# Performance work log

Hardware: AMD Instinct MI355X
Metric: run time of the kernel (lower is better)

The kernel has to match this reference:

```python
import jax, jax.numpy as jnp
import numpy as np

N_NODES = 100_000
N_EDGES = 1_600_000
N_GRAPHS = 512
IN_C, HID_C, OUT_C = 17, 64, 32


def setup_inputs() -> dict:
    key = jax.random.key(0)
    ks = jax.random.split(key, 12)
    x = jax.random.normal(ks[0], (N_NODES, IN_C), dtype=jnp.float32)
    edge_index = jax.random.randint(ks[1], (2, N_EDGES), 0, N_NODES, dtype=jnp.int64)
    batch = jnp.sort(jax.random.randint(ks[2], (N_NODES,), 0, N_GRAPHS, dtype=jnp.int64))
    def lin(k, fan_in, fan_out):
        s = 1.0 / np.sqrt(fan_in)
        kw, kb = jax.random.split(k)
        W = jax.random.uniform(kw, (fan_in, fan_out), minval=-s, maxval=s, dtype=jnp.float32)
        b = jax.random.uniform(kb, (fan_out,), minval=-s, maxval=s, dtype=jnp.float32)
        return W, b
    W1, b1 = lin(ks[3], IN_C, HID_C)      # GCNConv 1
    W2, b2 = lin(ks[4], HID_C, OUT_C)     # GCNConv 2
    Wf1, bf1 = lin(ks[5], OUT_C, OUT_C)   # fc1
    Wf2, bf2 = lin(ks[6], OUT_C, OUT_C)   # fc2
    return {"x": x, "edge_index": edge_index, "batch": batch,
            "W1": W1, "b1": b1, "W2": W2, "b2": b2,
            "Wf1": Wf1, "bf1": bf1, "Wf2": Wf2, "bf2": bf2}


def _gcn_conv(x, src, dst, norm, W, b, n_nodes):
    # PyG GCNConv: h = x @ W; out_i = sum_{j->i} norm_ij * h_j; out += bias
    h = x @ W                                   # [N, d_out]
    msg = h[src] * norm[:, None]                # gather + scale [E+N, d_out]
    out = jax.ops.segment_sum(msg, dst, num_segments=n_nodes)
    return out + b


def reference(x, edge_index, batch, W1, b1, W2, b2, Wf1, bf1, Wf2, bf2):
    n = x.shape[0]
    loops = jnp.arange(n, dtype=edge_index.dtype)
    src = jnp.concatenate([edge_index[0], loops])  # add self loops
    dst = jnp.concatenate([edge_index[1], loops])
    # symmetric normalization: deg^-1/2[src] * deg^-1/2[dst]
    deg = jax.ops.segment_sum(jnp.ones_like(dst, dtype=x.dtype), dst, num_segments=n)
    dinv = jnp.where(deg > 0, 1.0 / jnp.sqrt(deg), 0.0)
    norm = dinv[src] * dinv[dst]

    h = jax.nn.relu(_gcn_conv(x, src, dst, norm, W1, b1, n))
    h = _gcn_conv(h, src, dst, norm, W2, b2, n)

    # global mean pool over graphs
    cnt = jax.ops.segment_sum(jnp.ones((n,), dtype=h.dtype), batch, num_segments=N_GRAPHS)
    pooled = jax.ops.segment_sum(h, batch, num_segments=N_GRAPHS) / jnp.clip(cnt, 1.0)[:, None]

    out = jax.nn.relu(pooled @ Wf1 + bf1)
    out = out @ Wf2 + bf2
    return out  # [N_GRAPHS, OUT_C]
```

## Files before the change

### kernel.cpp

```cpp
#include <hip/hip_runtime.h>

#define IN_C 17
#define HID  64
#define OUTC 32

#define CH   8192
#define TA   512
#define NBP  512
#define BCAP 5632
#define BS_BLKS 8

typedef __attribute__((ext_vector_type(2))) float f2;
typedef __attribute__((ext_vector_type(8))) short bf16x8;
typedef __attribute__((ext_vector_type(4))) float f32x4;
__device__ __forceinline__ f2 mkf2(float x, float y) { f2 r; r.x = x; r.y = y; return r; }

__device__ __forceinline__ unsigned short f2bf(float f) {
    unsigned u = __float_as_uint(f);
    u += 0x7fffu + ((u >> 16) & 1u);
    return (unsigned short)(u >> 16);
}
__device__ __forceinline__ float bflo(unsigned u) { return __uint_as_float(u << 16); }
__device__ __forceinline__ float bfhi(unsigned u) { return __uint_as_float(u & 0xffff0000u); }

__global__ __launch_bounds__(TA) void k_binA(const int* __restrict__ src,
        const int* __restrict__ dst, int E,
        int* __restrict__ outbuf, int* __restrict__ cntmat, int* __restrict__ offmat,
        const float* __restrict__ W2, uint4* __restrict__ w2frag,
        float* __restrict__ pool, int poolN) {
    __shared__ int cnt[NBP];
    __shared__ int off[NBP];
    __shared__ int stage[CH];
    int t = threadIdx.x;
    for (int i = (int)(blockIdx.x * TA + t); i < poolN; i += (int)(gridDim.x * TA))
        pool[i] = 0.f;
    if (blockIdx.x == 0 && t < 256) {
        int f = t >> 6, l = t & 63;
        int kt = f >> 1, nt = f & 1;
        int kbase = kt * 32 + (l >> 4) * 8;
        int c = nt * 16 + (l & 15);
        unsigned short v[8];
#pragma unroll
        for (int j = 0; j < 8; ++j) v[j] = f2bf(W2[(kbase + j) * OUTC + c]);
        uint4 o;
        o.x = (unsigned)v[0] | ((unsigned)v[1] << 16);
        o.y = (unsigned)v[2] | ((unsigned)v[3] << 16);
        o.z = (unsigned)v[4] | ((unsigned)v[5] << 16);
        o.w = (unsigned)v[6] | ((unsigned)v[7] << 16);
        w2frag[f * 64 + l] = o;
    }
    long base = (long)blockIdx.x * CH;
    int nE = (int)(E - base); if (nE > CH) nE = CH;
    cnt[t] = 0;
    __syncthreads();
    int bk[16], pk[16], rk[16];
#pragma unroll
    for (int j = 0; j < 16; ++j) {
        int idx = t + j * TA;
        if (idx < nE) {
            long e = base + idx;
            int d = __builtin_nontemporal_load(&dst[e]);
            int s = __builtin_nontemporal_load(&src[e]);
            int b = d >> 8;
            bk[j] = b;
            pk[j] = s | ((d & 255) << 17);
            rk[j] = atomicAdd(&cnt[b], 1);
        } else bk[j] = -1;
    }
    __syncthreads();
    int c = cnt[t];
    off[t] = c;
    __syncthreads();
    int inc = c;
    for (int s = 1; s < NBP; s <<= 1) {
        int add = (t >= s) ? off[t - s] : 0;
        __syncthreads();
        inc += add; off[t] = inc;
        __syncthreads();
    }
    int excl = inc - c;
    __syncthreads();
    off[t] = excl;
    __syncthreads();
#pragma unroll
    for (int j = 0; j < 16; ++j)
        if (bk[j] >= 0) stage[off[bk[j]] + rk[j]] = pk[j];
    __syncthreads();
    for (int i = t; i < nE; i += TA) outbuf[base + i] = stage[i];
    cntmat[blockIdx.x * NBP + t] = c;
    offmat[blockIdx.x * NBP + t] = excl;
}

__global__ __launch_bounds__(NBP) void k_bsum1(const int* __restrict__ cntmat,
        int nblkA, int* __restrict__ part) {
    int t = threadIdx.x, b = blockIdx.x;
    int per = (nblkA + BS_BLKS - 1) / BS_BLKS;
    int i0 = b * per, i1 = min(i0 + per, nblkA);
    int s = 0;
    for (int i = i0; i < i1; ++i) s += cntmat[i * NBP + t];
    part[b * NBP + t] = s;
}

__global__ __launch_bounds__(NBP) void k_bsum2(const int* __restrict__ part,
        int* __restrict__ bbase) {
    __shared__ int sh[NBP];
    int t = threadIdx.x;
    int s = 0;
#pragma unroll
    for (int i = 0; i < BS_BLKS; ++i) s += part[i * NBP + t];
    sh[t] = s;
    __syncthreads();
    int inc = s;
    for (int st = 1; st < NBP; st <<= 1) {
        int add = (t >= st) ? sh[t - st] : 0;
        __syncthreads();
        inc += add; sh[t] = inc;
        __syncthreads();
    }
    bbase[t] = inc - s;
}

__global__ __launch_bounds__(TA) void k_binB(const int* __restrict__ outbuf,
        const int* __restrict__ cntmat, const int* __restrict__ offmat,
        const int* __restrict__ bbase, int nblkA, int N,
        int* __restrict__ csr, int2* __restrict__ meta,
        const float* __restrict__ x, unsigned* __restrict__ xs16h,
        unsigned short* __restrict__ xs17h) {
    __shared__ int segc[256], sego[256], segs[256];
    __shared__ int ndeg[256], noff[256];
    __shared__ int stage[BCAP];
    int t = threadIdx.x, b = blockIdx.x;
    if (t < 256) {
        int cc = 0, ss = 0;
        if (t < nblkA) { cc = cntmat[t * NBP + b]; ss = offmat[t * NBP + b]; }
        segc[t] = cc; segs[t] = ss; sego[t] = cc;
        ndeg[t] = 0;
    }
    __syncthreads();
    {
        int c = (t < 256) ? sego[t] : 0;
        int inc = c;
        for (int s = 1; s < 256; s <<= 1) {
            int add = (t < 256 && t >= s) ? sego[t - s] : 0;
            __syncthreads();
            if (t < 256) { inc += add; sego[t] = inc; }
            __syncthreads();
        }
        if (t < 256) sego[t] = inc - c;
    }
    __syncthreads();
    int wave = t >> 6, lane = t & 63;
    for (int i = wave; i < nblkA; i += TA / 64) {
        int c = segc[i], so = sego[i];
        long gs = (long)i * CH + segs[i];
        for (int l = lane; l < c; l += 64) {
            int p = so + l;
            if (p < BCAP) stage[p] = __builtin_nontemporal_load(&outbuf[gs + l]);
        }
    }
    __syncthreads();
    int T = sego[255] + segc[255];
    if (T > BCAP) T = BCAP;
    int mypk[11], myrk[11], ne = 0;
    for (int k = t; k < T; k += TA) {
        int p = stage[k];
        int l = (p >> 17) & 255;
        myrk[ne] = atomicAdd(&ndeg[l], 1);
        mypk[ne] = p;
        ne++;
    }
    __syncthreads();
    {
        int c = (t < 256) ? ndeg[t] : 0;
        if (t < 256) noff[t] = c;
        __syncthreads();
        int inc = c;
        for (int s = 1; s < 256; s <<= 1) {
            int add = (t < 256 && t >= s) ? noff[t - s] : 0;
            __syncthreads();
            if (t < 256) { inc += add; noff[t] = inc; }
            __syncthreads();
        }
        if (t < 256) noff[t] = inc - c;
    }
    __syncthreads();
    int gb = bbase[b];
    int n0 = b << 8;
    if (t < 256 && n0 + t < N) {
        int n = n0 + t;
        meta[n] = make_int2(gb + noff[t], ndeg[t]);
        float dinv = rsqrtf((float)(ndeg[t] + 1));
        const float* xr = x + (size_t)n * IN_C;
        unsigned* xo = xs16h + (size_t)n * 8;
#pragma unroll
        for (int w2 = 0; w2 < 8; ++w2) {
            unsigned lo = f2bf(xr[2 * w2] * dinv);
            unsigned hi = f2bf(xr[2 * w2 + 1] * dinv);
            xo[w2] = lo | (hi << 16);
        }
        xs17h[n] = f2bf(xr[16] * dinv);
    }
    for (int j = 0; j < ne; ++j) {
        int p = mypk[j];
        int l = (p >> 17) & 255;
        csr[gb + noff[l] + myrk[j]] = p & 0x1FFFF;
    }
}

__global__ __launch_bounds__(256) void k_gather1(
        const uint4* __restrict__ xs16v, const unsigned short* __restrict__ xs17h,
        const int* __restrict__ csr, const int2* __restrict__ meta,
        const float* __restrict__ W1, const float* __restrict__ b1,
        const uint4* __restrict__ w2frag, unsigned char* __restrict__ hs2b, int N) {
    __shared__ __align__(16) float aggx[16][20];
    __shared__ float dinv_sh[16];
    __shared__ __align__(16) float h1sh[16][68];

    int tid = threadIdx.x;
    int n0 = blockIdx.x * 16;
    int ch = tid & 63;
    float w1r[IN_C];
#pragma unroll
    for (int k = 0; k < IN_C; ++k) w1r[k] = W1[k * HID + ch];
    float b1v = b1[ch];

    int ln = tid >> 4, sl = tid & 15;
    int n = n0 + ln;
    f2 acc[8];
#pragma unroll
    for (int j = 0; j < 8; ++j) acc[j] = mkf2(0.f, 0.f);
    float a17 = 0.f;
    if (n < N) {
        int2 m = meta[n];
        int start = m.x, cnt = m.y, end = start + cnt;
        auto body = [&](int s) {
            uint4 v0 = xs16v[(size_t)s * 2];
            uint4 v1 = xs16v[(size_t)s * 2 + 1];
            acc[0] += mkf2(bflo(v0.x), bfhi(v0.x));
            acc[1] += mkf2(bflo(v0.y), bfhi(v0.y));
            acc[2] += mkf2(bflo(v0.z), bfhi(v0.z));
            acc[3] += mkf2(bflo(v0.w), bfhi(v0.w));
            acc[4] += mkf2(bflo(v1.x), bfhi(v1.x));
            acc[5] += mkf2(bflo(v1.y), bfhi(v1.y));
            acc[6] += mkf2(bflo(v1.z), bfhi(v1.z));
            acc[7] += mkf2(bflo(v1.w), bfhi(v1.w));
            a17 += bflo((unsigned)xs17h[s]);
        };
        for (int k = start + sl; k < end; k += 16)
            body(__builtin_nontemporal_load(&csr[k]));
        if (sl == 0) {
            body(n);
            dinv_sh[ln] = rsqrtf((float)(cnt + 1));
        }
    }
    float a[16];
#pragma unroll
    for (int j = 0; j < 8; ++j) { a[2 * j] = acc[j].x; a[2 * j + 1] = acc[j].y; }
#pragma unroll
    for (int j = 0; j < 8; ++j) {
        float tt = (sl & 8) ? a[j + 8] : a[j];
        float uu = (sl & 8) ? a[j] : a[j + 8];
        a[j] = tt + __shfl_xor(uu, 8);
    }
#pragma unroll
    for (int j = 0; j < 4; ++j) {
        float tt = (sl & 4) ? a[j + 4] : a[j];
        float uu = (sl & 4) ? a[j] : a[j + 4];
        a[j] = tt + __shfl_xor(uu, 4);
    }
#pragma unroll
    for (int j = 0; j < 2; ++j) {
        float tt = (sl & 2) ? a[j + 2] : a[j];
        float uu = (sl & 2) ? a[j] : a[j + 2];
        a[j] = tt + __shfl_xor(uu, 2);
    }
    {
        float tt = (sl & 1) ? a[1] : a[0];
        float uu = (sl & 1) ? a[0] : a[1];
        a[0] = tt + __shfl_xor(uu, 1);
    }
    a17 += __shfl_xor(a17, 1);
    a17 += __shfl_xor(a17, 2);
    a17 += __shfl_xor(a17, 4);
    a17 += __shfl_xor(a17, 8);
    aggx[ln][sl] = a[0];
    if (sl == 0) aggx[ln][16] = a17;
    __syncthreads();
    int s0 = tid >> 6;
#pragma unroll
    for (int rep = 0; rep < 4; ++rep) {
        int slot = s0 + rep * 4;
        int nn = n0 + slot;
        if (nn < N) {
            const float4* ap = (const float4*)aggx[slot];
            float4 A0 = ap[0], A1 = ap[1], A2 = ap[2], A3 = ap[3];
            float a16 = aggx[slot][16];
            float dot = A0.x * w1r[0]  + A0.y * w1r[1]  + A0.z * w1r[2]  + A0.w * w1r[3]
                      + A1.x * w1r[4]  + A1.y * w1r[5]  + A1.z * w1r[6]  + A1.w * w1r[7]
                      + A2.x * w1r[8]  + A2.y * w1r[9]  + A2.z * w1r[10] + A2.w * w1r[11]
                      + A3.x * w1r[12] + A3.y * w1r[13] + A3.z * w1r[14] + A3.w * w1r[15]
                      + a16  * w1r[16];
            float dv = dinv_sh[slot];
            h1sh[slot][ch] = dv * fmaxf(dv * dot + b1v, 0.f);
        }
    }
    __syncthreads();
    int wv = tid >> 6, l = tid & 63;
    if (wv < 2) {
        int row = l & 15, kq = l >> 4;
        const float4* hp = (const float4*)&h1sh[row][kq * 8];
        float4 f0v = hp[0], f1v = hp[1];
        const float4* hq = (const float4*)&h1sh[row][32 + kq * 8];
        float4 g0v = hq[0], g1v = hq[1];
        bf16x8 a0, a1;
        a0[0] = (short)f2bf(f0v.x); a0[1] = (short)f2bf(f0v.y);
        a0[2] = (short)f2bf(f0v.z); a0[3] = (short)f2bf(f0v.w);
        a0[4] = (short)f2bf(f1v.x); a0[5] = (short)f2bf(f1v.y);
        a0[6] = (short)f2bf(f1v.z); a0[7] = (short)f2bf(f1v.w);
        a1[0] = (short)f2bf(g0v.x); a1[1] = (short)f2bf(g0v.y);
        a1[2] = (short)f2bf(g0v.z); a1[3] = (short)f2bf(g0v.w);
        a1[4] = (short)f2bf(g1v.x); a1[5] = (short)f2bf(g1v.y);
        a1[6] = (short)f2bf(g1v.z); a1[7] = (short)f2bf(g1v.w);
        bf16x8 bA = *(const bf16x8*)&w2frag[(0 + wv) * 64 + l];
        bf16x8 bB = *(const bf16x8*)&w2frag[(2 + wv) * 64 + l];
        f32x4 d = {0.f, 0.f, 0.f, 0.f};
        d = __builtin_amdgcn_mfma_f32_16x16x32_bf16(a0, bA, d, 0, 0, 0);
        d = __builtin_amdgcn_mfma_f32_16x16x32_bf16(a1, bB, d, 0, 0, 0);
        int rbase = (l >> 4) * 4;
#pragma unroll
        for (int r = 0; r < 4; ++r) {
            int node = n0 + rbase + r;
            if (node < N) {
                unsigned pk = (unsigned)__builtin_amdgcn_cvt_pk_fp8_f32(d[r], 0.f, 0, false);
                hs2b[(size_t)node * 32 + wv * 16 + (l & 15)] = (unsigned char)(pk & 0xFFu);
            }
        }
    }
}

__global__ __launch_bounds__(256) void k_gather2(
        const uint4* __restrict__ hs2v, const int* __restrict__ csr,
        const int2* __restrict__ meta, const float* __restrict__ b2,
        const int* __restrict__ batch, float* pool, float* cntg, int N) {
    __shared__ __align__(16) float cont[16][OUTC];
    __shared__ int bsh[16];
    int tid = threadIdx.x;
    int n0 = blockIdx.x * 16;

    int ln = tid >> 4, sl = tid & 15;
    int n = n0 + ln;
    f2 acc[16];
#pragma unroll
    for (int j = 0; j < 16; ++j) acc[j] = mkf2(0.f, 0.f);
    float dinv = 0.f;
    if (n < N) {
        int2 m = meta[n];
        int start = m.x, cnt = m.y, end = start + cnt;
        dinv = rsqrtf((float)(cnt + 1));
        auto body = [&](int s) {
            const uint4* rp = hs2v + (size_t)s * 2;
            uint4 v0 = rp[0], v1 = rp[1];
            f2 t;
            t = __builtin_amdgcn_cvt_pk_f32_fp8((int)v0.x, false); acc[0]  += t;
            t = __builtin_amdgcn_cvt_pk_f32_fp8((int)v0.x, true);  acc[1]  += t;
            t = __builtin_amdgcn_cvt_pk_f32_fp8((int)v0.y, false); acc[2]  += t;
            t = __builtin_amdgcn_cvt_pk_f32_fp8((int)v0.y, true);  acc[3]  += t;
            t = __builtin_amdgcn_cvt_pk_f32_fp8((int)v0.z, false); acc[4]  += t;
            t = __builtin_amdgcn_cvt_pk_f32_fp8((int)v0.z, true);  acc[5]  += t;
            t = __builtin_amdgcn_cvt_pk_f32_fp8((int)v0.w, false); acc[6]  += t;
            t = __builtin_amdgcn_cvt_pk_f32_fp8((int)v0.w, true);  acc[7]  += t;
            t = __builtin_amdgcn_cvt_pk_f32_fp8((int)v1.x, false); acc[8]  += t;
            t = __builtin_amdgcn_cvt_pk_f32_fp8((int)v1.x, true);  acc[9]  += t;
            t = __builtin_amdgcn_cvt_pk_f32_fp8((int)v1.y, false); acc[10] += t;
            t = __builtin_amdgcn_cvt_pk_f32_fp8((int)v1.y, true);  acc[11] += t;
            t = __builtin_amdgcn_cvt_pk_f32_fp8((int)v1.z, false); acc[12] += t;
            t = __builtin_amdgcn_cvt_pk_f32_fp8((int)v1.z, true);  acc[13] += t;
            t = __builtin_amdgcn_cvt_pk_f32_fp8((int)v1.w, false); acc[14] += t;
            t = __builtin_amdgcn_cvt_pk_f32_fp8((int)v1.w, true);  acc[15] += t;
        };
        for (int k = start + sl; k < end; k += 16)
            body(__builtin_nontemporal_load(&csr[k]));
        if (sl == 0) body(n);
    }
    float a[32];
#pragma unroll
    for (int j = 0; j < 16; ++j) { a[2 * j] = acc[j].x; a[2 * j + 1] = acc[j].y; }
#pragma unroll
    for (int j = 0; j < 16; ++j) {
        float tt = (sl & 8) ? a[j + 16] : a[j];
        float uu = (sl & 8) ? a[j] : a[j + 16];
        a[j] = tt + __shfl_xor(uu, 8);
    }
#pragma unroll
    for (int j = 0; j < 8; ++j) {
        float tt = (sl & 4) ? a[j + 8] : a[j];
        float uu = (sl & 4) ? a[j] : a[j + 8];
        a[j] = tt + __shfl_xor(uu, 4);
    }
#pragma unroll
    for (int j = 0; j < 4; ++j) {
        float tt = (sl & 2) ? a[j + 4] : a[j];
        float uu = (sl & 2) ? a[j] : a[j + 4];
        a[j] = tt + __shfl_xor(uu, 2);
    }
#pragma unroll
    for (int j = 0; j < 2; ++j) {
        float tt = (sl & 1) ? a[j + 2] : a[j];
        float uu = (sl & 1) ? a[j] : a[j + 2];
        a[j] = tt + __shfl_xor(uu, 1);
    }
    if (n < N) {
        float c0 = dinv * a[0] + b2[2 * sl];
        float c1 = dinv * a[1] + b2[2 * sl + 1];
        *(float2*)&cont[ln][2 * sl] = make_float2(c0, c1);
        if (sl == 0) bsh[ln] = batch[n];
    } else {
        *(float2*)&cont[ln][2 * sl] = make_float2(0.f, 0.f);
        if (sl == 0) bsh[ln] = -1;
    }
    __syncthreads();
    if (tid < OUTC) {
        int c = tid;
        float run = 0.f; int cur = -1;
        for (int j = 0; j < 16; ++j) {
            int bj = bsh[j];
            if (bj < 0) continue;
            if (bj == cur) run += cont[j][c];
            else {
                if (cur >= 0) atomicAdd(&pool[(size_t)cur * OUTC + c], run);
                cur = bj; run = cont[j][c];
            }
        }
        if (cur >= 0) atomicAdd(&pool[(size_t)cur * OUTC + c], run);
        if (c == 0) {
            float crun = 0.f; cur = -1;
            for (int j = 0; j < 16; ++j) {
                int bj = bsh[j];
                if (bj < 0) continue;
                if (bj == cur) crun += 1.f;
                else {
                    if (cur >= 0) atomicAdd(&cntg[cur], crun);
                    cur = bj; crun = 1.f;
                }
            }
            if (cur >= 0) atomicAdd(&cntg[cur], crun);
        }
    }
}

__global__ void k_final(const float* __restrict__ pool, const float* __restrict__ cntg,
                        const float* __restrict__ Wf1, const float* __restrict__ bf1,
                        const float* __restrict__ Wf2, const float* __restrict__ bf2,
                        float* out, int G) {
    __shared__ float p[OUTC], t[OUTC];
    int g = blockIdx.x;
    int c = threadIdx.x;
    float csafe = fmaxf(cntg[g], 1.0f);
    p[c] = pool[g * OUTC + c] / csafe;
    __syncthreads();
    float acc = bf1[c];
#pragma unroll
    for (int k = 0; k < OUTC; ++k) acc += p[k] * Wf1[k * OUTC + c];
    t[c] = fmaxf(acc, 0.f);
    __syncthreads();
    float acc2 = bf2[c];
#pragma unroll
    for (int k = 0; k < OUTC; ++k) acc2 += t[k] * Wf2[k * OUTC + c];
    out[g * OUTC + c] = acc2;
}

extern "C" void kernel_launch(void* const* d_in, const int* in_sizes, int n_in,
                              void* d_out, int out_size, void* d_ws, size_t ws_size,
                              hipStream_t stream) {
    const float* x    = (const float*)d_in[0];
    const int*   ei   = (const int*)  d_in[1];
    const int*   batch= (const int*)  d_in[2];
    const float* W1   = (const float*)d_in[3];
    const float* b1   = (const float*)d_in[4];
    const float* W2   = (const float*)d_in[5];
    const float* b2   = (const float*)d_in[6];
    const float* Wf1  = (const float*)d_in[7];
    const float* bf1  = (const float*)d_in[8];
    const float* Wf2  = (const float*)d_in[9];
    const float* bf2  = (const float*)d_in[10];

    const int N = in_sizes[0] / IN_C;
    const int E = in_sizes[1] / 2;
    const int G = out_size / OUTC;
    const int* src = ei;
    const int* dst = ei + E;

    const int nblkA = (E + CH - 1) / CH;
    const int NB    = (N + 255) >> 8;

    char* w = (char*)d_ws;
    int*   csr      = (int*)w;   w += (size_t)E * sizeof(int);
    int2*  meta     = (int2*)w;  w += (size_t)N * sizeof(int2);
    unsigned* xs16h = (unsigned*)w; w += (size_t)N * 8 * sizeof(unsigned);
    unsigned char* hs2 = (unsigned char*)w; w += (size_t)N * 32;
    unsigned short* xs17h = (unsigned short*)w; w += (size_t)N * sizeof(unsigned short);
    w = (char*)(((size_t)w + 15) & ~(size_t)15);
    float* pool     = (float*)w; w += (size_t)G * OUTC * sizeof(float);
    float* cntg     = (float*)w; w += (size_t)G * sizeof(float);
    w = (char*)(((size_t)w + 15) & ~(size_t)15);
    int*   outbuf   = (int*)w;   w += (size_t)E * sizeof(int);
    int*   cntmat   = (int*)w;   w += (size_t)nblkA * NBP * sizeof(int);
    int*   offmat   = (int*)w;   w += (size_t)nblkA * NBP * sizeof(int);
    int*   bbase    = (int*)w;   w += NBP * sizeof(int);
    int*   part     = (int*)w;   w += BS_BLKS * NBP * sizeof(int);
    w = (char*)(((size_t)w + 15) & ~(size_t)15);
    uint4* w2frag   = (uint4*)w; w += 4 * 64 * sizeof(uint4);

    const int poolN = G * OUTC + G;

    k_binA<<<nblkA, TA, 0, stream>>>(src, dst, E, outbuf, cntmat, offmat,
                                     W2, w2frag, pool, poolN);
    k_bsum1<<<BS_BLKS, NBP, 0, stream>>>(cntmat, nblkA, part);
    k_bsum2<<<1, NBP, 0, stream>>>(part, bbase);
    k_binB<<<NB, TA, 0, stream>>>(outbuf, cntmat, offmat, bbase, nblkA, N,
                                  csr, meta, x, xs16h, xs17h);

    dim3 blk(256);
    k_gather1<<<(N + 15) / 16, blk, 0, stream>>>((const uint4*)xs16h, xs17h, csr, meta,
                                                 W1, b1, w2frag, hs2, N);

    k_gather2<<<(N + 15) / 16, blk, 0, stream>>>((const uint4*)hs2, csr, meta,
                                                 b2, batch, pool, cntg, N);

    k_final<<<G, OUTC, 0, stream>>>(pool, cntg, Wf1, bf1, Wf2, bf2, (float*)d_out, G);
}
```

Before: 121.2 us.

## Process 64 nodes per block with 4 lanes per node in both gather kernels

```diff
diff --git a/kernel.cpp b/kernel.cpp
--- a/kernel.cpp
+++ b/kernel.cpp
@@ -212,19 +212,19 @@
         const int* __restrict__ csr, const int2* __restrict__ meta,
         const float* __restrict__ W1, const float* __restrict__ b1,
         const uint4* __restrict__ w2frag, unsigned char* __restrict__ hs2b, int N) {
-    __shared__ __align__(16) float aggx[16][20];
-    __shared__ float dinv_sh[16];
-    __shared__ __align__(16) float h1sh[16][68];
+    __shared__ __align__(16) float aggx[64][20];
+    __shared__ float dinv_sh[64];
+    __shared__ __align__(16) float h1sh[64][68];
 
     int tid = threadIdx.x;
-    int n0 = blockIdx.x * 16;
+    int n0 = blockIdx.x * 64;
     int ch = tid & 63;
     float w1r[IN_C];
 #pragma unroll
     for (int k = 0; k < IN_C; ++k) w1r[k] = W1[k * HID + ch];
     float b1v = b1[ch];
 
-    int ln = tid >> 4, sl = tid & 15;
+    int ln = tid >> 2, sl = tid & 3;
     int n = n0 + ln;
     f2 acc[8];
 #pragma unroll
@@ -246,8 +246,13 @@
             acc[7] += mkf2(bflo(v1.w), bfhi(v1.w));
             a17 += bflo((unsigned)xs17h[s]);
         };
-        for (int k = start + sl; k < end; k += 16)
-            body(__builtin_nontemporal_load(&csr[k]));
+        int k = start + sl;
+        for (; k + 4 < end; k += 8) {
+            int s0e = __builtin_nontemporal_load(&csr[k]);
+            int s1e = __builtin_nontemporal_load(&csr[k + 4]);
+            body(s0e); body(s1e);
+        }
+        if (k < end) body(__builtin_nontemporal_load(&csr[k]));
         if (sl == 0) {
             body(n);
             dinv_sh[ln] = rsqrtf((float)(cnt + 1));
@@ -258,38 +263,25 @@
     for (int j = 0; j < 8; ++j) { a[2 * j] = acc[j].x; a[2 * j + 1] = acc[j].y; }
 #pragma unroll
     for (int j = 0; j < 8; ++j) {
-        float tt = (sl & 8) ? a[j + 8] : a[j];
-        float uu = (sl & 8) ? a[j] : a[j + 8];
-        a[j] = tt + __shfl_xor(uu, 8);
+        float tt = (sl & 2) ? a[j + 8] : a[j];
+        float uu = (sl & 2) ? a[j] : a[j + 8];
+        a[j] = tt + __shfl_xor(uu, 2);
     }
 #pragma unroll
     for (int j = 0; j < 4; ++j) {
-        float tt = (sl & 4) ? a[j + 4] : a[j];
-        float uu = (sl & 4) ? a[j] : a[j + 4];
-        a[j] = tt + __shfl_xor(uu, 4);
-    }
-#pragma unroll
-    for (int j = 0; j < 2; ++j) {
-        float tt = (sl & 2) ? a[j + 2] : a[j];
-        float uu = (sl & 2) ? a[j] : a[j + 2];
-        a[j] = tt + __shfl_xor(uu, 2);
-    }
-    {
-        float tt = (sl & 1) ? a[1] : a[0];
-        float uu = (sl & 1) ? a[0] : a[1];
-        a[0] = tt + __shfl_xor(uu, 1);
+        float tt = (sl & 1) ? a[j + 4] : a[j];
+        float uu = (sl & 1) ? a[j] : a[j + 4];
+        a[j] = tt + __shfl_xor(uu, 1);
     }
     a17 += __shfl_xor(a17, 1);
     a17 += __shfl_xor(a17, 2);
-    a17 += __shfl_xor(a17, 4);
-    a17 += __shfl_xor(a17, 8);
-    aggx[ln][sl] = a[0];
+    *(float4*)&aggx[ln][sl * 4] = make_float4(a[0], a[1], a[2], a[3]);
     if (sl == 0) aggx[ln][16] = a17;
     __syncthreads();
-    int s0 = tid >> 6;
-#pragma unroll
-    for (int rep = 0; rep < 4; ++rep) {
-        int slot = s0 + rep * 4;
+    int w0 = tid >> 6;
+#pragma unroll
+    for (int rep = 0; rep < 16; ++rep) {
+        int slot = w0 + rep * 4;
         int nn = n0 + slot;
         if (nn < N) {
             const float4* ap = (const float4*)aggx[slot];
@@ -306,11 +298,12 @@
     }
     __syncthreads();
     int wv = tid >> 6, l = tid & 63;
-    if (wv < 2) {
+    {
         int row = l & 15, kq = l >> 4;
-        const float4* hp = (const float4*)&h1sh[row][kq * 8];
+        int rbase16 = wv * 16;
+        const float4* hp = (const float4*)&h1sh[rbase16 + row][kq * 8];
         float4 f0v = hp[0], f1v = hp[1];
-        const float4* hq = (const float4*)&h1sh[row][32 + kq * 8];
+        const float4* hq = (const float4*)&h1sh[rbase16 + row][32 + kq * 8];
         float4 g0v = hq[0], g1v = hq[1];
         bf16x8 a0, a1;
         a0[0] = (short)f2bf(f0v.x); a0[1] = (short)f2bf(f0v.y);
@@ -321,18 +314,24 @@
         a1[2] = (short)f2bf(g0v.z); a1[3] = (short)f2bf(g0v.w);
         a1[4] = (short)f2bf(g1v.x); a1[5] = (short)f2bf(g1v.y);
         a1[6] = (short)f2bf(g1v.z); a1[7] = (short)f2bf(g1v.w);
-        bf16x8 bA = *(const bf16x8*)&w2frag[(0 + wv) * 64 + l];
-        bf16x8 bB = *(const bf16x8*)&w2frag[(2 + wv) * 64 + l];
-        f32x4 d = {0.f, 0.f, 0.f, 0.f};
-        d = __builtin_amdgcn_mfma_f32_16x16x32_bf16(a0, bA, d, 0, 0, 0);
-        d = __builtin_amdgcn_mfma_f32_16x16x32_bf16(a1, bB, d, 0, 0, 0);
-        int rbase = (l >> 4) * 4;
+        bf16x8 b00 = *(const bf16x8*)&w2frag[0 * 64 + l];
+        bf16x8 b01 = *(const bf16x8*)&w2frag[1 * 64 + l];
+        bf16x8 b10 = *(const bf16x8*)&w2frag[2 * 64 + l];
+        bf16x8 b11 = *(const bf16x8*)&w2frag[3 * 64 + l];
+        f32x4 d0 = {0.f, 0.f, 0.f, 0.f}, d1 = {0.f, 0.f, 0.f, 0.f};
+        d0 = __builtin_amdgcn_mfma_f32_16x16x32_bf16(a0, b00, d0, 0, 0, 0);
+        d0 = __builtin_amdgcn_mfma_f32_16x16x32_bf16(a1, b10, d0, 0, 0, 0);
+        d1 = __builtin_amdgcn_mfma_f32_16x16x32_bf16(a0, b01, d1, 0, 0, 0);
+        d1 = __builtin_amdgcn_mfma_f32_16x16x32_bf16(a1, b11, d1, 0, 0, 0);
+        int rb = (l >> 4) * 4;
 #pragma unroll
         for (int r = 0; r < 4; ++r) {
-            int node = n0 + rbase + r;
+            int node = n0 + rbase16 + rb + r;
             if (node < N) {
-                unsigned pk = (unsigned)__builtin_amdgcn_cvt_pk_fp8_f32(d[r], 0.f, 0, false);
-                hs2b[(size_t)node * 32 + wv * 16 + (l & 15)] = (unsigned char)(pk & 0xFFu);
+                unsigned p0 = (unsigned)__builtin_amdgcn_cvt_pk_fp8_f32(d0[r], 0.f, 0, false);
+                unsigned p1 = (unsigned)__builtin_amdgcn_cvt_pk_fp8_f32(d1[r], 0.f, 0, false);
+                hs2b[(size_t)node * 32 + (l & 15)]      = (unsigned char)(p0 & 0xFFu);
+                hs2b[(size_t)node * 32 + 16 + (l & 15)] = (unsigned char)(p1 & 0xFFu);
             }
         }
     }
@@ -342,12 +341,12 @@
         const uint4* __restrict__ hs2v, const int* __restrict__ csr,
         const int2* __restrict__ meta, const float* __restrict__ b2,
         const int* __restrict__ batch, float* pool, float* cntg, int N) {
-    __shared__ __align__(16) float cont[16][OUTC];
-    __shared__ int bsh[16];
+    __shared__ __align__(16) float cont[64][OUTC];
+    __shared__ int bsh[64];
     int tid = threadIdx.x;
-    int n0 = blockIdx.x * 16;
-
-    int ln = tid >> 4, sl = tid & 15;
+    int n0 = blockIdx.x * 64;
+
+    int ln = tid >> 2, sl = tid & 3;
     int n = n0 + ln;
     f2 acc[16];
 #pragma unroll
@@ -378,8 +377,13 @@
             t = __builtin_amdgcn_cvt_pk_f32_fp8((int)v1.w, false); acc[14] += t;
             t = __builtin_amdgcn_cvt_pk_f32_fp8((int)v1.w, true);  acc[15] += t;
         };
-        for (int k = start + sl; k < end; k += 16)
-            body(__builtin_nontemporal_load(&csr[k]));
+        int k = start + sl;
+        for (; k + 4 < end; k += 8) {
+            int s0e = __builtin_nontemporal_load(&csr[k]);
+            int s1e = __builtin_nontemporal_load(&csr[k + 4]);
+            body(s0e); body(s1e);
+        }
+        if (k < end) body(__builtin_nontemporal_load(&csr[k]));
         if (sl == 0) body(n);
     }
     float a[32];
@@ -387,42 +391,38 @@
     for (int j = 0; j < 16; ++j) { a[2 * j] = acc[j].x; a[2 * j + 1] = acc[j].y; }
 #pragma unroll
     for (int j = 0; j < 16; ++j) {
-        float tt = (sl & 8) ? a[j + 16] : a[j];
-        float uu = (sl & 8) ? a[j] : a[j + 16];
-        a[j] = tt + __shfl_xor(uu, 8);
+        float tt = (sl & 2) ? a[j + 16] : a[j];
+        float uu = (sl & 2) ? a[j] : a[j + 16];
+        a[j] = tt + __shfl_xor(uu, 2);
     }
 #pragma unroll
     for (int j = 0; j < 8; ++j) {
-        float tt = (sl & 4) ? a[j + 8] : a[j];
-        float uu = (sl & 4) ? a[j] : a[j + 8];
-        a[j] = tt + __shfl_xor(uu, 4);
-    }
-#pragma unroll
-    for (int j = 0; j < 4; ++j) {
-        float tt = (sl & 2) ? a[j + 4] : a[j];
-        float uu = (sl & 2) ? a[j] : a[j + 4];
-        a[j] = tt + __shfl_xor(uu, 2);
-    }
-#pragma unroll
-    for (int j = 0; j < 2; ++j) {
-        float tt = (sl & 1) ? a[j + 2] : a[j];
-        float uu = (sl & 1) ? a[j] : a[j + 2];
+        float tt = (sl & 1) ? a[j + 8] : a[j];
+        float uu = (sl & 1) ? a[j] : a[j + 8];
         a[j] = tt + __shfl_xor(uu, 1);
     }
     if (n < N) {
-        float c0 = dinv * a[0] + b2[2 * sl];
-        float c1 = dinv * a[1] + b2[2 * sl + 1];
-        *(float2*)&cont[ln][2 * sl] = make_float2(c0, c1);
+        float c0 = dinv * a[0] + b2[sl * 8 + 0];
+        float c1 = dinv * a[1] + b2[sl * 8 + 1];
+        float c2 = dinv * a[2] + b2[sl * 8 + 2];
+        float c3 = dinv * a[3] + b2[sl * 8 + 3];
+        float c4 = dinv * a[4] + b2[sl * 8 + 4];
+        float c5 = dinv * a[5] + b2[sl * 8 + 5];
+        float c6 = dinv * a[6] + b2[sl * 8 + 6];
+        float c7 = dinv * a[7] + b2[sl * 8 + 7];
+        *(float4*)&cont[ln][sl * 8]     = make_float4(c0, c1, c2, c3);
+        *(float4*)&cont[ln][sl * 8 + 4] = make_float4(c4, c5, c6, c7);
         if (sl == 0) bsh[ln] = batch[n];
     } else {
-        *(float2*)&cont[ln][2 * sl] = make_float2(0.f, 0.f);
+        *(float4*)&cont[ln][sl * 8]     = make_float4(0.f, 0.f, 0.f, 0.f);
+        *(float4*)&cont[ln][sl * 8 + 4] = make_float4(0.f, 0.f, 0.f, 0.f);
         if (sl == 0) bsh[ln] = -1;
     }
     __syncthreads();
     if (tid < OUTC) {
         int c = tid;
         float run = 0.f; int cur = -1;
-        for (int j = 0; j < 16; ++j) {
+        for (int j = 0; j < 64; ++j) {
             int bj = bsh[j];
             if (bj < 0) continue;
             if (bj == cur) run += cont[j][c];
@@ -434,7 +434,7 @@
         if (cur >= 0) atomicAdd(&pool[(size_t)cur * OUTC + c], run);
         if (c == 0) {
             float crun = 0.f; cur = -1;
-            for (int j = 0; j < 16; ++j) {
+            for (int j = 0; j < 64; ++j) {
                 int bj = bsh[j];
                 if (bj < 0) continue;
                 if (bj == cur) crun += 1.f;
@@ -521,10 +521,10 @@
                                   csr, meta, x, xs16h, xs17h);
 
     dim3 blk(256);
-    k_gather1<<<(N + 15) / 16, blk, 0, stream>>>((const uint4*)xs16h, xs17h, csr, meta,
+    k_gather1<<<(N + 63) / 64, blk, 0, stream>>>((const uint4*)xs16h, xs17h, csr, meta,
                                                  W1, b1, w2frag, hs2, N);
 
-    k_gather2<<<(N + 15) / 16, blk, 0, stream>>>((const uint4*)hs2, csr, meta,
+    k_gather2<<<(N + 63) / 64, blk, 0, stream>>>((const uint4*)hs2, csr, meta,
                                                  b2, batch, pool, cntg, N);
 
     k_final<<<G, OUTC, 0, stream>>>(pool, cntg, Wf1, bf1, Wf2, bf2, (float*)d_out, G);
```

Result: no change. 123.2 us (+1.6%).
